# Kernel optimization log

Hardware: AMD Instinct MI355X
Metric: run time of the kernel (lower is better)

Reference implementation:

```python
import jax, jax.numpy as jnp
import numpy as np

N_NODES = 50000
N_EDGES = 400000
DIMS = 32
HEADS = 6
FEAT = DIMS * HEADS  # 192
NEG_SLOPE = 0.2  # PyG GATv2Conv default


def glorot(key, shape):
    fan_in, fan_out = shape[0], shape[1]
    lim = jnp.sqrt(6.0 / (fan_in + fan_out))
    return jax.random.uniform(key, shape, jnp.float32, -lim, lim)


def setup_inputs() -> dict:
    key = jax.random.key(0)
    ks = jax.random.split(key, 10)
    x = jax.random.normal(ks[0], (N_NODES, FEAT), jnp.float32)
    edge_index = jax.random.randint(ks[1], (2, N_EDGES), 0, N_NODES, jnp.int32)
    edge_weights = jax.random.uniform(ks[2], (N_EDGES, 1), jnp.float32)
    W_l = glorot(ks[3], (FEAT, FEAT))   # lin_l: in -> heads*out
    b_l = jnp.zeros((FEAT,), jnp.float32)
    W_r = glorot(ks[4], (FEAT, FEAT))   # lin_r (share_weights=False)
    b_r = jnp.zeros((FEAT,), jnp.float32)
    W_edge = glorot(ks[5], (1, FEAT))   # lin_edge: edge_dim=1 -> heads*out, no bias
    att = glorot(ks[6], (HEADS, DIMS))  # attention vector per head
    bias = jnp.zeros((FEAT,), jnp.float32)
    return {"x": x, "edge_index": edge_index, "edge_weights": edge_weights,
            "W_l": W_l, "b_l": b_l, "W_r": W_r, "b_r": b_r,
            "W_edge": W_edge, "att": att, "bias": bias}


def gatv2_res(x, edge_index, edge_weights, W_l, b_l, W_r, b_r, W_edge, att, bias):
    N = x.shape[0]
    H, C = att.shape
    src0, dst0 = edge_index[0], edge_index[1]

    # add_self_loops with fill_value='mean': self-loop attr = mean of edge_attr over incoming edges
    cnt = jax.ops.segment_sum(jnp.ones((edge_weights.shape[0],), x.dtype), dst0, num_segments=N)
    loop_attr = jax.ops.segment_sum(edge_weights, dst0, num_segments=N) / jnp.maximum(cnt, 1.0)[:, None]
    loops = jnp.arange(N, dtype=src0.dtype)
    src = jnp.concatenate([src0, loops])
    dst = jnp.concatenate([dst0, loops])
    e_attr = jnp.concatenate([edge_weights, loop_attr], axis=0)  # [E+N, 1]

    x_l = (x @ W_l + b_l).reshape(N, H, C)  # source transform
    x_r = (x @ W_r + b_r).reshape(N, H, C)  # target transform
    e_emb = (e_attr @ W_edge).reshape(-1, H, C)

    # per-edge GATv2 score
    m = jax.nn.leaky_relu(x_l[src] + x_r[dst] + e_emb, NEG_SLOPE)  # [E+N, H, C]
    alpha = jnp.einsum('ehc,hc->eh', m, att)  # [E+N, H]

    # segment softmax over edges incident to each target node (self-loops guarantee coverage)
    amax = jax.lax.stop_gradient(jax.ops.segment_max(alpha, dst, num_segments=N))
    ex = jnp.exp(alpha - amax[dst])
    denom = jax.ops.segment_sum(ex, dst, num_segments=N)
    a = ex / denom[dst]  # [E+N, H]

    out = jax.ops.segment_sum(x_l[src] * a[..., None], dst, num_segments=N)  # [N, H, C]
    out = out.reshape(N, H * C) + bias

    # ResLayer: residual + ReLU (dropout = identity in eval mode)
    return jax.nn.relu(x + out)


def reference(x, edge_index, edge_weights, W_l, b_l, W_r, b_r, W_edge, att, bias):
    return gatv2_res(x, edge_index, edge_weights, W_l, b_l, W_r, b_r, W_edge, att, bias)
```

## Files before the change

### kernel.cpp

```cpp
#include <hip/hip_runtime.h>
#include <hip/hip_bf16.h>
#include <math.h>

#define N_NODES 50000
#define N_EDGES 400000
#define HEADS 6
#define DIMS 32
#define FEAT 192
#define NEG_SLOPE 0.2f

typedef __attribute__((ext_vector_type(8))) short short8;
typedef __attribute__((ext_vector_type(4))) float f32x4;

__device__ __forceinline__ unsigned short f2bu(float f) {
    __hip_bfloat16 h = __float2bfloat16(f);
    unsigned short u; __builtin_memcpy(&u, &h, 2); return u;
}
__device__ __forceinline__ float bu2f(unsigned short u) {
    return __uint_as_float(((unsigned)u) << 16);
}

#define XL_OFF    0
#define XR_OFF    19200000
#define WT_OFF    38400000
#define BLR_OFF   38547456
#define PAIR_OFF  38548992
#define DEG_OFF   41748992
#define SCAN_OFF  41948992
#define BSUM_OFF  42148992
#define BOFF_OFF  42150016
#define NB_SCAN ((N_NODES + 255) / 256)

__global__ __launch_bounds__(256) void k_count(const int* __restrict__ ei,
                                               int* __restrict__ deg,
                                               const float* __restrict__ Wl,
                                               const float* __restrict__ Wr,
                                               const float* __restrict__ bl,
                                               const float* __restrict__ br,
                                               short* __restrict__ Wt,
                                               float* __restrict__ blr) {
    int e = blockIdx.x * blockDim.x + threadIdx.x;
    if (e < N_EDGES) atomicAdd(&deg[ei[N_EDGES + e]], 1);
    if (e < 384 * FEAT) {
        int n = e / FEAT, k = e - n * FEAT;
        float v = (n < FEAT) ? Wl[k * FEAT + n] : Wr[k * FEAT + (n - FEAT)];
        Wt[n * FEAT + k] = (short)f2bu(v);
    }
    if (e < 384) blr[e] = (e < FEAT) ? bl[e] : br[e - FEAT];
}

__global__ __launch_bounds__(256) void k_scan1(const int* __restrict__ deg,
                                               int* __restrict__ scan,
                                               int* __restrict__ bsums) {
    int t = threadIdx.x;
    int i = blockIdx.x * 256 + t;
    int v = (i < N_NODES) ? deg[i] : 0;
    __shared__ int s[256];
    s[t] = v; __syncthreads();
    for (int off = 1; off < 256; off <<= 1) {
        int u = (t >= off) ? s[t - off] : 0;
        __syncthreads();
        s[t] += u;
        __syncthreads();
    }
    if (i < N_NODES) scan[i] = s[t];
    if (t == 255) bsums[blockIdx.x] = s[255];
}

__global__ __launch_bounds__(256) void k_scan2(int* __restrict__ bsums,
                                               int* __restrict__ boffs) {
    int t = threadIdx.x;
    int v = (t < NB_SCAN) ? bsums[t] : 0;
    __shared__ int s[256];
    s[t] = v; __syncthreads();
    for (int off = 1; off < 256; off <<= 1) {
        int u = (t >= off) ? s[t - off] : 0;
        __syncthreads();
        s[t] += u;
        __syncthreads();
    }
    boffs[t] = s[t] - v;
}

#define SCAT_BLOCKS ((N_EDGES + 383) / 384)
#define GEMM_BLOCKS (N_NODES / 16)
#define OSTRIDE 392
#define ASTRIDE 200
__global__ __launch_bounds__(384) void k_scatgemm(const int* __restrict__ ei,
                                                  const float* __restrict__ ew,
                                                  const int* __restrict__ scan,
                                                  const int* __restrict__ boffs,
                                                  int* __restrict__ deg,
                                                  int2* __restrict__ pair,
                                                  const float* __restrict__ x,
                                                  const short* __restrict__ Wt,
                                                  const float* __restrict__ blr,
                                                  unsigned short* __restrict__ xl,
                                                  unsigned short* __restrict__ xr) {
    __shared__ unsigned short sOut[16 * OSTRIDE];
    __shared__ unsigned short sA[16 * ASTRIDE];
    if (blockIdx.x < SCAT_BLOCKS) {
        int e = blockIdx.x * 384 + threadIdx.x;
        if (e < N_EDGES) {
            int d = ei[N_EDGES + e];
            int inclEnd = boffs[d >> 8] + scan[d];
            int old = atomicSub(&deg[d], 1);
            int2 p; p.x = ei[e]; p.y = __float_as_int(ew[e]);
            pair[inclEnd - old] = p;
        }
        return;
    }
    size_t row0 = (size_t)(blockIdx.x - SCAT_BLOCKS) * 16;

    {
        int q = threadIdx.x;
        int row = q / 24, k0 = (q - row * 24) * 8;
        const float* ap = x + (row0 + row) * FEAT + k0;
        float4 v0 = *(const float4*)ap;
        float4 v1 = *(const float4*)(ap + 4);
        unsigned short tmp[8];
        tmp[0] = f2bu(v0.x); tmp[1] = f2bu(v0.y); tmp[2] = f2bu(v0.z); tmp[3] = f2bu(v0.w);
        tmp[4] = f2bu(v1.x); tmp[5] = f2bu(v1.y); tmp[6] = f2bu(v1.z); tmp[7] = f2bu(v1.w);
        int kw = (k0 >> 1) ^ ((row & 7) << 2);
        *(uint4*)&sA[row * ASTRIDE + kw * 2] = *(const uint4*)tmp;
    }
    __syncthreads();

    int wv   = threadIdx.x >> 6;
    int lane = threadIdx.x & 63;
    int m    = lane & 15;
    int kg   = lane >> 4;
    int ncol0 = wv * 64;

    f32x4 acc0 = {0.f,0.f,0.f,0.f}, acc1 = acc0, acc2 = acc0, acc3 = acc0;

#pragma unroll
    for (int ks = 0; ks < 6; ks++) {
        int kb = ks * 32 + kg * 8;
        int kw = (kb >> 1) ^ ((m & 7) << 2);
        short8 af = *(const short8*)&sA[m * ASTRIDE + kw * 2];
        const short* wp = Wt + (size_t)(ncol0 + m) * FEAT + kb;
        short8 b0 = *(const short8*)(wp);
        short8 b1 = *(const short8*)(wp + 16 * FEAT);
        short8 b2 = *(const short8*)(wp + 32 * FEAT);
        short8 b3 = *(const short8*)(wp + 48 * FEAT);
        acc0 = __builtin_amdgcn_mfma_f32_16x16x32_bf16(af, b0, acc0, 0, 0, 0);
        acc1 = __builtin_amdgcn_mfma_f32_16x16x32_bf16(af, b1, acc1, 0, 0, 0);
        acc2 = __builtin_amdgcn_mfma_f32_16x16x32_bf16(af, b2, acc2, 0, 0, 0);
        acc3 = __builtin_amdgcn_mfma_f32_16x16x32_bf16(af, b3, acc3, 0, 0, 0);
    }

    f32x4 accs[4] = {acc0, acc1, acc2, acc3};
#pragma unroll
    for (int t4 = 0; t4 < 4; t4++) {
        int cc = ncol0 + t4 * 16 + m;
        float bv = blr[cc];
#pragma unroll
        for (int r = 0; r < 4; r++) {
            sOut[(kg * 4 + r) * OSTRIDE + cc] = f2bu(accs[t4][r] + bv);
        }
    }
    __syncthreads();
    for (int q = threadIdx.x; q < 768; q += 384) {
        int row = q / 48, p = q - row * 48;
        uint4 v = *(const uint4*)&sOut[row * OSTRIDE + p * 8];
        if (p < 24) *(uint4*)(xl + (row0 + row) * FEAT + p * 8) = v;
        else        *(uint4*)(xr + (row0 + row) * FEAT + (p - 24) * 8) = v;
    }
}

#define NPB 8
#define CEDGE 32
#define RS 100
__global__ __launch_bounds__(192) void k_node(const float* __restrict__ x,
                                              const float* __restrict__ bias,
                                              const float* __restrict__ att,
                                              const float* __restrict__ We,
                                              const int* __restrict__ scan,
                                              const int* __restrict__ boffs,
                                              const int2* __restrict__ pair,
                                              const unsigned short* __restrict__ xl,
                                              const unsigned short* __restrict__ xr,
                                              float* __restrict__ out) {
    __shared__ __align__(16) unsigned int sXL[CEDGE * RS];
    __shared__ __align__(16) unsigned int sXR[NPB * RS];
    __shared__ __align__(16) unsigned int sXS[NPB * RS];
    __shared__ float sEx[CEDGE * HEADS];
    __shared__ float sExS[NPB * HEADS];
    __shared__ int   sSrc[CEDGE];
    __shared__ float sW[CEDGE];
    __shared__ int   sDst[CEDGE];
    __shared__ int   sStart[NPB + 1];
    __shared__ float sAttP[HEADS * 33], sWeP[HEADS * 33];

    int t = threadIdx.x;
    int h = t >> 5;
    int n0 = blockIdx.x * NPB;

    for (int q = t; q < HEADS * 33; q += 192) {
        int hh = q / 33, c = q - hh * 33;
        if (c < 32) { sAttP[q] = att[hh * 32 + c]; sWeP[q] = We[hh * 32 + c]; }
    }
    if (t <= NPB) {
        int n = n0 + t;
        int st;
        if (n >= N_NODES) st = N_EDGES;
        else {
            int b = n >> 8;
            st = boffs[b] + ((n & 255) ? scan[n - 1] : 0);
        }
        sStart[t] = st;
    }
    {
        int nn = t / 24, p = t - nn * 24;
        *(uint4*)&sXR[nn * RS + p * 4] = ((const uint4*)(xr + (size_t)(n0 + nn) * FEAT))[p];
        *(uint4*)&sXS[nn * RS + p * 4] = ((const uint4*)(xl + (size_t)(n0 + nn) * FEAT))[p];
    }
    __syncthreads();

    int gbase = sStart[0];
    int etot = sStart[NPB] - gbase;
    float acc[NPB], den[NPB], wsm[NPB];
#pragma unroll
    for (int nn = 0; nn < NPB; nn++) { acc[nn] = 0.f; den[nn] = 0.f; wsm[nn] = 0.f; }

    for (int i0 = 0; i0 < etot; i0 += CEDGE) {
        int c = etot - i0; if (c > CEDGE) c = CEDGE;
        if (t < c) {
            int2 p = pair[gbase + i0 + t];
            sSrc[t] = p.x;
            sW[t] = __int_as_float(p.y);
        }
        if (t < NPB) {
            int lo = sStart[t] - gbase - i0;     if (lo < 0) lo = 0;
            int hi = sStart[t + 1] - gbase - i0; if (hi > c) hi = c;
            for (int q = lo; q < hi; q++) sDst[q] = t;
        }
        __syncthreads();
        int nld = c * 24;
#pragma unroll
        for (int s = 0; s < 4; s++) {
            int q = t + s * 192;
            if (q < nld) {
                int i = q / 24, p = q - i * 24;
                *(uint4*)&sXL[i * RS + p * 4] =
                    *(const uint4*)(xl + (size_t)sSrc[i] * FEAT + p * 8);
            }
        }
        __syncthreads();
        if (t < c * HEADS) {
            int i = t / HEADS, hh = t - i * HEADS;
            int nn = sDst[i];
            float w = sW[i];
            const uint4* pa = (const uint4*)&sXL[i * RS + hh * 16];
            const uint4* pb = (const uint4*)&sXR[nn * RS + hh * 16];
            float alpha = 0.f;
#pragma unroll
            for (int g = 0; g < 4; g++) {
                uint4 a4 = pa[g];
                uint4 b4 = pb[g];
                unsigned aw[4] = {a4.x, a4.y, a4.z, a4.w};
                unsigned bw[4] = {b4.x, b4.y, b4.z, b4.w};
#pragma unroll
                for (int q = 0; q < 4; q++) {
                    int c0 = g * 8 + q * 2;
                    float m0 = bu2f((unsigned short)aw[q]) + bu2f((unsigned short)bw[q]) + w * sWeP[hh * 33 + c0];
                    m0 = (m0 > 0.f) ? m0 : NEG_SLOPE * m0;
                    alpha += m0 * sAttP[hh * 33 + c0];
                    float m1 = bu2f((unsigned short)(aw[q] >> 16)) + bu2f((unsigned short)(bw[q] >> 16)) + w * sWeP[hh * 33 + c0 + 1];
                    m1 = (m1 > 0.f) ? m1 : NEG_SLOPE * m1;
                    alpha += m1 * sAttP[hh * 33 + c0 + 1];
                }
            }
            sEx[t] = __expf(alpha);
        }
        __syncthreads();
        {
            int cw = t >> 1;
#pragma unroll
            for (int nn = 0; nn < NPB; nn++) {
                int lo = sStart[nn] - gbase - i0;     if (lo < 0) lo = 0;
                int hi = sStart[nn + 1] - gbase - i0; if (hi > c) hi = c;
                for (int i = lo; i < hi; i++) {
                    float ex = sEx[i * HEADS + h];
                    unsigned u = sXL[i * RS + cw];
                    unsigned short v = (t & 1) ? (unsigned short)(u >> 16) : (unsigned short)u;
                    acc[nn] += ex * bu2f(v);
                    den[nn] += ex;
                    wsm[nn] += sW[i];
                }
            }
        }
        __syncthreads();
    }

    if (t < NPB * HEADS) {
        int nn = t / HEADS, hh = t - nn * HEADS;
        int dg = sStart[nn + 1] - sStart[nn];
        float w = wsm[nn] / fmaxf((float)dg, 1.0f);
        const uint4* pa = (const uint4*)&sXS[nn * RS + hh * 16];
        const uint4* pb = (const uint4*)&sXR[nn * RS + hh * 16];
        float alpha = 0.f;
#pragma unroll
        for (int g = 0; g < 4; g++) {
            uint4 a4 = pa[g];
            uint4 b4 = pb[g];
            unsigned aw[4] = {a4.x, a4.y, a4.z, a4.w};
            unsigned bw[4] = {b4.x, b4.y, b4.z, b4.w};
#pragma unroll
            for (int q = 0; q < 4; q++) {
                int c0 = g * 8 + q * 2;
                float m0 = bu2f((unsigned short)aw[q]) + bu2f((unsigned short)bw[q]) + w * sWeP[hh * 33 + c0];
                m0 = (m0 > 0.f) ? m0 : NEG_SLOPE * m0;
                alpha += m0 * sAttP[hh * 33 + c0];
                float m1 = bu2f((unsigned short)(aw[q] >> 16)) + bu2f((unsigned short)(bw[q] >> 16)) + w * sWeP[hh * 33 + c0 + 1];
                m1 = (m1 > 0.f) ? m1 : NEG_SLOPE * m1;
                alpha += m1 * sAttP[hh * 33 + c0 + 1];
            }
        }
        sExS[t] = __expf(alpha);
    }
    __syncthreads();

    float bj = bias[t];
    int cw = t >> 1;
#pragma unroll
    for (int nn = 0; nn < NPB; nn++) {
        float exS = sExS[nn * HEADS + h];
        unsigned u = sXS[nn * RS + cw];
        unsigned short v = (t & 1) ? (unsigned short)(u >> 16) : (unsigned short)u;
        float num = acc[nn] + exS * bu2f(v);
        float dn  = den[nn] + exS;
        size_t off = (size_t)(n0 + nn) * FEAT + t;
        float val = x[off] + bj + num / dn;
        out[off] = (val > 0.f) ? val : 0.f;
    }
}

extern "C" void kernel_launch(void* const* d_in, const int* in_sizes, int n_in,
                              void* d_out, int out_size, void* d_ws, size_t ws_size,
                              hipStream_t stream) {
    const float* x    = (const float*)d_in[0];
    const int*   ei   = (const int*)d_in[1];
    const float* ew   = (const float*)d_in[2];
    const float* Wl   = (const float*)d_in[3];
    const float* bl   = (const float*)d_in[4];
    const float* Wr   = (const float*)d_in[5];
    const float* br   = (const float*)d_in[6];
    const float* We   = (const float*)d_in[7];
    const float* att  = (const float*)d_in[8];
    const float* bias = (const float*)d_in[9];
    float* out = (float*)d_out;

    char* ws = (char*)d_ws;
    unsigned short* xl = (unsigned short*)(ws + XL_OFF);
    unsigned short* xr = (unsigned short*)(ws + XR_OFF);
    short* Wt     = (short*)(ws + WT_OFF);
    float* blr    = (float*)(ws + BLR_OFF);
    int2*  pair   = (int2*)(ws + PAIR_OFF);
    int*   deg    = (int*)(ws + DEG_OFF);
    int*   scan   = (int*)(ws + SCAN_OFF);
    int*   bsums  = (int*)(ws + BSUM_OFF);
    int*   boffs  = (int*)(ws + BOFF_OFF);

    hipMemsetAsync(ws + DEG_OFF, 0, N_NODES * sizeof(int), stream);

    k_count<<<(N_EDGES + 255) / 256, 256, 0, stream>>>(ei, deg, Wl, Wr, bl, br, Wt, blr);
    k_scan1<<<NB_SCAN, 256, 0, stream>>>(deg, scan, bsums);
    k_scan2<<<1, 256, 0, stream>>>(bsums, boffs);

    k_scatgemm<<<SCAT_BLOCKS + GEMM_BLOCKS, 384, 0, stream>>>(ei, ew, scan, boffs, deg,
                                                              pair, x, Wt, blr, xl, xr);

    k_node<<<N_NODES / NPB, 192, 0, stream>>>(x, bias, att, We, scan, boffs,
                                              pair, xl, xr, out);
}
```

Before: 283.8 us.

## Double-buffer edge gathers in node kernel and precompute per-node edge-weight sums

```diff
diff --git a/kernel.cpp b/kernel.cpp
--- a/kernel.cpp
+++ b/kernel.cpp
@@ -26,13 +26,16 @@
 #define BLR_OFF   38547456
 #define PAIR_OFF  38548992
 #define DEG_OFF   41748992
-#define SCAN_OFF  41948992
-#define BSUM_OFF  42148992
-#define BOFF_OFF  42150016
+#define WSUM_OFF  41948992
+#define SCAN_OFF  42148992
+#define BSUM_OFF  42348992
+#define BOFF_OFF  42350016
 #define NB_SCAN ((N_NODES + 255) / 256)
 
 __global__ __launch_bounds__(256) void k_count(const int* __restrict__ ei,
+                                               const float* __restrict__ ew,
                                                int* __restrict__ deg,
+                                               float* __restrict__ wsum,
                                                const float* __restrict__ Wl,
                                                const float* __restrict__ Wr,
                                                const float* __restrict__ bl,
@@ -40,7 +43,11 @@
                                                short* __restrict__ Wt,
                                                float* __restrict__ blr) {
     int e = blockIdx.x * blockDim.x + threadIdx.x;
-    if (e < N_EDGES) atomicAdd(&deg[ei[N_EDGES + e]], 1);
+    if (e < N_EDGES) {
+        int d = ei[N_EDGES + e];
+        atomicAdd(&deg[d], 1);
+        unsafeAtomicAdd(&wsum[d], ew[e]);
+    }
     if (e < 384 * FEAT) {
         int n = e / FEAT, k = e - n * FEAT;
         float v = (n < FEAT) ? Wl[k * FEAT + n] : Wr[k * FEAT + (n - FEAT)];
@@ -178,24 +185,37 @@
                                               const float* __restrict__ We,
                                               const int* __restrict__ scan,
                                               const int* __restrict__ boffs,
+                                              const float* __restrict__ wsum,
                                               const int2* __restrict__ pair,
                                               const unsigned short* __restrict__ xl,
                                               const unsigned short* __restrict__ xr,
                                               float* __restrict__ out) {
-    __shared__ __align__(16) unsigned int sXL[CEDGE * RS];
+    __shared__ __align__(16) unsigned int sXL[2][CEDGE * RS];
     __shared__ __align__(16) unsigned int sXR[NPB * RS];
     __shared__ __align__(16) unsigned int sXS[NPB * RS];
     __shared__ float sEx[CEDGE * HEADS];
     __shared__ float sExS[NPB * HEADS];
-    __shared__ int   sSrc[CEDGE];
-    __shared__ float sW[CEDGE];
-    __shared__ int   sDst[CEDGE];
+    __shared__ int   sSrc[2][CEDGE];
+    __shared__ float sW[2][CEDGE];
+    __shared__ int   sDst[2][CEDGE];
     __shared__ int   sStart[NPB + 1];
     __shared__ float sAttP[HEADS * 33], sWeP[HEADS * 33];
+    __shared__ float sDen[NPB * HEADS];
 
     int t = threadIdx.x;
     int h = t >> 5;
     int n0 = blockIdx.x * NPB;
+
+    int gbase = boffs[n0 >> 8] + ((n0 & 255) ? scan[n0 - 1] : 0);
+    int n8 = n0 + NPB;
+    int gend = (n8 >= N_NODES) ? N_EDGES
+             : (boffs[n8 >> 8] + ((n8 & 255) ? scan[n8 - 1] : 0));
+    int etot = gend - gbase;
+
+    int c0 = min(etot, CEDGE);
+    int c1 = min(etot - CEDGE, CEDGE);
+    if (t < c0) { int2 p = pair[gbase + t];          sSrc[0][t] = p.x; sW[0][t] = __int_as_float(p.y); }
+    if (t < c1) { int2 p = pair[gbase + CEDGE + t];  sSrc[1][t] = p.x; sW[1][t] = __int_as_float(p.y); }
 
     for (int q = t; q < HEADS * 33; q += 192) {
         int hh = q / 33, c = q - hh * 33;
@@ -218,41 +238,56 @@
     }
     __syncthreads();
 
-    int gbase = sStart[0];
-    int etot = sStart[NPB] - gbase;
-    float acc[NPB], den[NPB], wsm[NPB];
-#pragma unroll
-    for (int nn = 0; nn < NPB; nn++) { acc[nn] = 0.f; den[nn] = 0.f; wsm[nn] = 0.f; }
-
-    for (int i0 = 0; i0 < etot; i0 += CEDGE) {
-        int c = etot - i0; if (c > CEDGE) c = CEDGE;
-        if (t < c) {
-            int2 p = pair[gbase + i0 + t];
-            sSrc[t] = p.x;
-            sW[t] = __int_as_float(p.y);
-        }
-        if (t < NPB) {
-            int lo = sStart[t] - gbase - i0;     if (lo < 0) lo = 0;
-            int hi = sStart[t + 1] - gbase - i0; if (hi > c) hi = c;
-            for (int q = lo; q < hi; q++) sDst[q] = t;
-        }
-        __syncthreads();
-        int nld = c * 24;
+    if (t < NPB) {
+        int lo = sStart[t] - gbase;     if (lo < 0) lo = 0;
+        int hi = sStart[t + 1] - gbase; if (hi > c0) hi = c0;
+        for (int q = lo; q < hi; q++) sDst[0][q] = t;
+    }
+    {
+        int nld = c0 * 24;
 #pragma unroll
         for (int s = 0; s < 4; s++) {
             int q = t + s * 192;
             if (q < nld) {
                 int i = q / 24, p = q - i * 24;
-                *(uint4*)&sXL[i * RS + p * 4] =
-                    *(const uint4*)(xl + (size_t)sSrc[i] * FEAT + p * 8);
-            }
-        }
-        __syncthreads();
+                *(uint4*)&sXL[0][i * RS + p * 4] =
+                    *(const uint4*)(xl + (size_t)sSrc[0][i] * FEAT + p * 8);
+            }
+        }
+    }
+
+    float acc[NPB];
+#pragma unroll
+    for (int nn = 0; nn < NPB; nn++) acc[nn] = 0.f;
+    float denR = 0.f;
+    int nnD = t / HEADS, hhD = t - nnD * HEADS;
+
+    int nch = (etot + CEDGE - 1) / CEDGE;
+    for (int ci = 0; ci < nch; ci++) {
+        __syncthreads();
+        int i0 = ci * CEDGE;
+        int c   = min(etot - i0, CEDGE);
+        int cn  = min(etot - i0 - CEDGE, CEDGE);
+        int cn2 = min(etot - i0 - 2 * CEDGE, CEDGE);
+        int cb = ci & 1, nb = cb ^ 1;
+
+        uint4 G0, G1, G2, G3;
+        int nldn = (cn > 0) ? cn * 24 : 0;
+        {
+            int q0 = t, q1 = t + 192, q2 = t + 384, q3 = t + 576;
+            if (q0 < nldn) { int i = q0 / 24, p = q0 - i * 24; G0 = *(const uint4*)(xl + (size_t)sSrc[nb][i] * FEAT + p * 8); }
+            if (q1 < nldn) { int i = q1 / 24, p = q1 - i * 24; G1 = *(const uint4*)(xl + (size_t)sSrc[nb][i] * FEAT + p * 8); }
+            if (q2 < nldn) { int i = q2 / 24, p = q2 - i * 24; G2 = *(const uint4*)(xl + (size_t)sSrc[nb][i] * FEAT + p * 8); }
+            if (q3 < nldn) { int i = q3 / 24, p = q3 - i * 24; G3 = *(const uint4*)(xl + (size_t)sSrc[nb][i] * FEAT + p * 8); }
+        }
+        int2 P;
+        if (t < cn2) P = pair[gbase + i0 + 2 * CEDGE + t];
+
         if (t < c * HEADS) {
             int i = t / HEADS, hh = t - i * HEADS;
-            int nn = sDst[i];
-            float w = sW[i];
-            const uint4* pa = (const uint4*)&sXL[i * RS + hh * 16];
+            int nn = sDst[cb][i];
+            float w = sW[cb][i];
+            const uint4* pa = (const uint4*)&sXL[cb][i * RS + hh * 16];
             const uint4* pb = (const uint4*)&sXR[nn * RS + hh * 16];
             float alpha = 0.f;
 #pragma unroll
@@ -263,13 +298,13 @@
                 unsigned bw[4] = {b4.x, b4.y, b4.z, b4.w};
 #pragma unroll
                 for (int q = 0; q < 4; q++) {
-                    int c0 = g * 8 + q * 2;
-                    float m0 = bu2f((unsigned short)aw[q]) + bu2f((unsigned short)bw[q]) + w * sWeP[hh * 33 + c0];
-                    m0 = (m0 > 0.f) ? m0 : NEG_SLOPE * m0;
-                    alpha += m0 * sAttP[hh * 33 + c0];
-                    float m1 = bu2f((unsigned short)(aw[q] >> 16)) + bu2f((unsigned short)(bw[q] >> 16)) + w * sWeP[hh * 33 + c0 + 1];
-                    m1 = (m1 > 0.f) ? m1 : NEG_SLOPE * m1;
-                    alpha += m1 * sAttP[hh * 33 + c0 + 1];
+                    int cc = g * 8 + q * 2;
+                    float m0 = bu2f((unsigned short)aw[q]) + bu2f((unsigned short)bw[q]) + w * sWeP[hh * 33 + cc];
+                    m0 = fmaxf(m0, NEG_SLOPE * m0);
+                    alpha += m0 * sAttP[hh * 33 + cc];
+                    float m1 = bu2f((unsigned short)(aw[q] >> 16)) + bu2f((unsigned short)(bw[q] >> 16)) + w * sWeP[hh * 33 + cc + 1];
+                    m1 = fmaxf(m1, NEG_SLOPE * m1);
+                    alpha += m1 * sAttP[hh * 33 + cc + 1];
                 }
             }
             sEx[t] = __expf(alpha);
@@ -283,21 +318,37 @@
                 int hi = sStart[nn + 1] - gbase - i0; if (hi > c) hi = c;
                 for (int i = lo; i < hi; i++) {
                     float ex = sEx[i * HEADS + h];
-                    unsigned u = sXL[i * RS + cw];
+                    unsigned u = sXL[cb][i * RS + cw];
                     unsigned short v = (t & 1) ? (unsigned short)(u >> 16) : (unsigned short)u;
                     acc[nn] += ex * bu2f(v);
-                    den[nn] += ex;
-                    wsm[nn] += sW[i];
                 }
             }
-        }
-        __syncthreads();
+            if (t < NPB * HEADS) {
+                int lo = sStart[nnD] - gbase - i0;     if (lo < 0) lo = 0;
+                int hi = sStart[nnD + 1] - gbase - i0; if (hi > c) hi = c;
+                for (int i = lo; i < hi; i++) denR += sEx[i * HEADS + hhD];
+            }
+            if (t < NPB && cn > 0) {
+                int lo = sStart[t] - gbase - i0 - CEDGE;     if (lo < 0) lo = 0;
+                int hi = sStart[t + 1] - gbase - i0 - CEDGE; if (hi > cn) hi = cn;
+                for (int q = lo; q < hi; q++) sDst[nb][q] = t;
+            }
+        }
+        {
+            int q0 = t, q1 = t + 192, q2 = t + 384, q3 = t + 576;
+            if (q0 < nldn) { int i = q0 / 24, p = q0 - i * 24; *(uint4*)&sXL[nb][i * RS + p * 4] = G0; }
+            if (q1 < nldn) { int i = q1 / 24, p = q1 - i * 24; *(uint4*)&sXL[nb][i * RS + p * 4] = G1; }
+            if (q2 < nldn) { int i = q2 / 24, p = q2 - i * 24; *(uint4*)&sXL[nb][i * RS + p * 4] = G2; }
+            if (q3 < nldn) { int i = q3 / 24, p = q3 - i * 24; *(uint4*)&sXL[nb][i * RS + p * 4] = G3; }
+        }
+        if (t < cn2) { sSrc[cb][t] = P.x; sW[cb][t] = __int_as_float(P.y); }
     }
 
     if (t < NPB * HEADS) {
-        int nn = t / HEADS, hh = t - nn * HEADS;
+        sDen[t] = denR;
+        int nn = nnD, hh = hhD;
         int dg = sStart[nn + 1] - sStart[nn];
-        float w = wsm[nn] / fmaxf((float)dg, 1.0f);
+        float w = wsum[n0 + nn] / fmaxf((float)dg, 1.0f);
         const uint4* pa = (const uint4*)&sXS[nn * RS + hh * 16];
         const uint4* pb = (const uint4*)&sXR[nn * RS + hh * 16];
         float alpha = 0.f;
@@ -309,13 +360,13 @@
             unsigned bw[4] = {b4.x, b4.y, b4.z, b4.w};
 #pragma unroll
             for (int q = 0; q < 4; q++) {
-                int c0 = g * 8 + q * 2;
-                float m0 = bu2f((unsigned short)aw[q]) + bu2f((unsigned short)bw[q]) + w * sWeP[hh * 33 + c0];
-                m0 = (m0 > 0.f) ? m0 : NEG_SLOPE * m0;
-                alpha += m0 * sAttP[hh * 33 + c0];
-                float m1 = bu2f((unsigned short)(aw[q] >> 16)) + bu2f((unsigned short)(bw[q] >> 16)) + w * sWeP[hh * 33 + c0 + 1];
-                m1 = (m1 > 0.f) ? m1 : NEG_SLOPE * m1;
-                alpha += m1 * sAttP[hh * 33 + c0 + 1];
+                int cc = g * 8 + q * 2;
+                float m0 = bu2f((unsigned short)aw[q]) + bu2f((unsigned short)bw[q]) + w * sWeP[hh * 33 + cc];
+                m0 = fmaxf(m0, NEG_SLOPE * m0);
+                alpha += m0 * sAttP[hh * 33 + cc];
+                float m1 = bu2f((unsigned short)(aw[q] >> 16)) + bu2f((unsigned short)(bw[q] >> 16)) + w * sWeP[hh * 33 + cc + 1];
+                m1 = fmaxf(m1, NEG_SLOPE * m1);
+                alpha += m1 * sAttP[hh * 33 + cc + 1];
             }
         }
         sExS[t] = __expf(alpha);
@@ -330,7 +381,7 @@
         unsigned u = sXS[nn * RS + cw];
         unsigned short v = (t & 1) ? (unsigned short)(u >> 16) : (unsigned short)u;
         float num = acc[nn] + exS * bu2f(v);
-        float dn  = den[nn] + exS;
+        float dn  = sDen[nn * HEADS + h] + exS;
         size_t off = (size_t)(n0 + nn) * FEAT + t;
         float val = x[off] + bj + num / dn;
         out[off] = (val > 0.f) ? val : 0.f;
@@ -359,19 +410,20 @@
     float* blr    = (float*)(ws + BLR_OFF);
     int2*  pair   = (int2*)(ws + PAIR_OFF);
     int*   deg    = (int*)(ws + DEG_OFF);
+    float* wsum   = (float*)(ws + WSUM_OFF);
     int*   scan   = (int*)(ws + SCAN_OFF);
     int*   bsums  = (int*)(ws + BSUM_OFF);
     int*   boffs  = (int*)(ws + BOFF_OFF);
 
-    hipMemsetAsync(ws + DEG_OFF, 0, N_NODES * sizeof(int), stream);
-
-    k_count<<<(N_EDGES + 255) / 256, 256, 0, stream>>>(ei, deg, Wl, Wr, bl, br, Wt, blr);
+    hipMemsetAsync(ws + DEG_OFF, 0, 2 * N_NODES * sizeof(int), stream);
+
+    k_count<<<(N_EDGES + 255) / 256, 256, 0, stream>>>(ei, ew, deg, wsum, Wl, Wr, bl, br, Wt, blr);
     k_scan1<<<NB_SCAN, 256, 0, stream>>>(deg, scan, bsums);
     k_scan2<<<1, 256, 0, stream>>>(bsums, boffs);
 
     k_scatgemm<<<SCAT_BLOCKS + GEMM_BLOCKS, 384, 0, stream>>>(ei, ew, scan, boffs, deg,
                                                               pair, x, Wt, blr, xl, xr);
 
-    k_node<<<N_NODES / NPB, 192, 0, stream>>>(x, bias, att, We, scan, boffs,
+    k_node<<<N_NODES / NPB, 192, 0, stream>>>(x, bias, att, We, scan, boffs, wsum,
                                               pair, xl, xr, out);
 }
```

Measured after the change: 320.8 us. 13.0% more time.
